# Kernel tuning notes

Hardware: AMD Instinct MI355X
Metric: run time of the kernel (lower is better)

## Reference

```python
import jax, jax.numpy as jnp
import numpy as np
from jax import lax

BN_EPS = 1e-5


def setup_inputs() -> dict:
    key = jax.random.key(0)
    ks = jax.random.split(key, 4)
    T, N, I, H, O, K = 2048, 16, 1024, 2048, 1024, 12
    return {
        "inputs": jax.random.normal(ks[0], (T, N, I), dtype=jnp.float32),
        "wv": jax.random.normal(ks[1], (H, I), dtype=jnp.float32) * (1.0 / np.sqrt(I)),
        "gamma": jnp.ones((H,), dtype=jnp.float32),
        "beta": jnp.zeros((H,), dtype=jnp.float32),
        "wu": jax.random.normal(ks[2], (O, H), dtype=jnp.float32) * (1.0 / np.sqrt(H)),
        "bu": jnp.zeros((O,), dtype=jnp.float32),
        "memory_weights": jax.random.normal(ks[3], (K, H), dtype=jnp.float32) * 0.05,
        "stride": 2,
        "l_memory_size": 10,
        "r_memory_size": 1,
    }


def _memory_block(p, memory_weights, stride, l_mem, r_mem):
    # p: [N, T, H]. p_hatt[n,t,h] = sum_k w[k,h] * p[n, t + (k-l_mem)*stride, h]
    # == depthwise 1D cross-correlation with dilation=stride, 'same' asymmetric pad.
    H = p.shape[-1]
    x = jnp.transpose(p, (0, 2, 1))              # [N, H, T]
    kern = memory_weights.T[:, None, :]          # [H, 1, K]
    out = lax.conv_general_dilated(
        x, kern,
        window_strides=(1,),
        padding=[(l_mem * stride, r_mem * stride)],
        rhs_dilation=(stride,),
        dimension_numbers=("NCH", "OIH", "NCH"),
        feature_group_count=H,
    )
    return jnp.transpose(out, (0, 2, 1))         # [N, T, H]


def reference(inputs, wv, gamma, beta, wu, bu, memory_weights,
              stride, l_memory_size, r_memory_size):
    # wx_v then transpose(0,1): [T,N,I] -> [N,T,H]
    p = jnp.einsum("tni,hi->nth", inputs, wv)
    p_hatt = p + _memory_block(p, memory_weights, stride, l_memory_size, r_memory_size)
    # SequenceWise(BatchNorm1d) in train mode: stats over flattened (N*T) rows.
    H = p_hatt.shape[-1]
    flat = p_hatt.reshape(-1, H)
    mean = flat.mean(axis=0)
    var = flat.var(axis=0)  # biased, matches torch BN normalization
    xn = (p_hatt - mean) * lax.rsqrt(var + BN_EPS) * gamma + beta
    h = jax.nn.relu(jnp.einsum("nth,oh->nto", xn, wu) + bu)
    return (h, p_hatt)
```

## Files before the change

### kernel.cpp

```cpp
#include <hip/hip_runtime.h>
#include <hip/hip_bf16.h>
#include <stdint.h>

#define T_DIM 2048
#define N_DIM 16
#define I_DIM 1024
#define H_DIM 2048
#define O_DIM 1024
#define K_TAPS 12
#define MROWS (N_DIM * T_DIM)
#define BN_EPS 1e-5f

#define S_LEN 1024
#define CSTEPS 16
#define CROWS 27
#define CGROUP 2

typedef __attribute__((ext_vector_type(8))) short bf16x8;
typedef __attribute__((ext_vector_type(4))) float f32x4;

__device__ __forceinline__ unsigned short f2bf_rne(float f) {
    union { float f; unsigned u; } v; v.f = f;
    unsigned u = v.u;
    unsigned r = u + 0x7fffu + ((u >> 16) & 1u);
    return (unsigned short)(r >> 16);
}

__device__ __forceinline__ float bf2f(unsigned short x) {
    union { unsigned u; float f; } v; v.u = ((unsigned)x) << 16; return v.f;
}

__global__ void cvt_kernel(const float* __restrict__ in, unsigned short* __restrict__ out, int n4) {
    int i = blockIdx.x * blockDim.x + threadIdx.x;
    int stride = gridDim.x * blockDim.x;
    for (; i < n4; i += stride) {
        float4 v = ((const float4*)in)[i];
        ushort4 o;
        o.x = f2bf_rne(v.x); o.y = f2bf_rne(v.y);
        o.z = f2bf_rne(v.z); o.w = f2bf_rne(v.w);
        ((ushort4*)out)[i] = o;
    }
}

__device__ __forceinline__ void gload_lds16(const void* g, void* l) {
    __builtin_amdgcn_global_load_lds(
        (const __attribute__((address_space(1))) unsigned int*)g,
        (__attribute__((address_space(3))) unsigned int*)l, 16, 0, 0);
}

template<int PERM, int EPI, int KD, int NCOLS>
__global__ __launch_bounds__(512, 2) void gemm256(
    const unsigned short* __restrict__ A,
    const unsigned short* __restrict__ B,
    void* __restrict__ Cout,
    const float* __restrict__ bias)
{
    __shared__ char lds[131072];

    const int tid  = threadIdx.x;
    const int wid  = tid >> 6;
    const int lane = tid & 63;
    const int wr   = (wid >> 2) * 128;
    const int wc   = (wid & 3) * 64;
    const int fr   = lane & 15;
    const int fh   = lane >> 4;

    const int nwg = gridDim.x;
    const int lin = blockIdx.x;
    const int tile = (lin & 7) * (nwg >> 3) + (lin >> 3);
    const int ntx = NCOLS / 256;
    const long c0 = (long)(tile % ntx) * 256;
    const long r0 = (long)(tile / ntx) * 256;

    long aBase, aStride;
    if (PERM) {
        const long n0 = r0 / T_DIM;
        const long t0 = r0 % T_DIM;
        aBase = (t0 * N_DIM + n0) * (long)KD;
        aStride = (long)N_DIM * KD;
    } else {
        aBase = r0 * (long)KD;
        aStride = KD;
    }
    const long bBase = c0 * (long)KD;

    auto stage_half = [&](int buf, int mat, int h, int kt) {
        char* mbase = lds + buf * 65536 + mat * 32768 + h * 16384;
#pragma unroll
        for (int j = 0; j < 2; ++j) {
            const int row = h * 128 + j * 64 + (tid >> 3);
            const int g   = (tid & 7) ^ (row & 7);
            long gelem;
            if (mat == 0) gelem = aBase + (long)row * aStride + (long)kt * 64 + g * 8;
            else          gelem = bBase + (long)row * (long)KD + (long)kt * 64 + g * 8;
            gload_lds16((const char*)(mat == 0 ? A : B) + gelem * 2,
                        mbase + j * 8192 + tid * 16);
        }
    };

    auto rdA = [&](int buf, int m, int ks) -> bf16x8 {
        const int row = wr + m * 16 + fr;
        const int blk = ks * 4 + fh;
        return *(const bf16x8*)(lds + buf * 65536 + row * 128 + ((blk ^ (row & 7)) << 4));
    };
    auto rdB = [&](int buf, int n, int ks) -> bf16x8 {
        const int row = wc + n * 16 + fr;
        const int blk = ks * 4 + fh;
        return *(const bf16x8*)(lds + buf * 65536 + 32768 + row * 128 + ((blk ^ (row & 7)) << 4));
    };

    f32x4 acc[8][4] = {};

    stage_half(0, 0, 0, 0); stage_half(0, 0, 1, 0);
    stage_half(0, 1, 0, 0); stage_half(0, 1, 1, 0);

    const int KT  = KD / 64;
    const int KT2 = KT / 2;
    for (int i = 0; i < KT2; ++i) {
        const int tB = 2 * i + 1;
        const bool haveNext = (i + 1 < KT2);
        bf16x8 bfr[4][2];

#pragma unroll
        for (int q = 0; q < 4; ++q) {
            stage_half(1, q >> 1, q & 1, tB);
            bf16x8 af[2][2];
            if (q == 0) {
                asm volatile("s_waitcnt vmcnt(2)" ::: "memory");
                __builtin_amdgcn_s_barrier();
#pragma unroll
                for (int n = 0; n < 4; ++n)
#pragma unroll
                    for (int ks = 0; ks < 2; ++ks) bfr[n][ks] = rdB(0, n, ks);
#pragma unroll
                for (int mm = 0; mm < 2; ++mm)
#pragma unroll
                    for (int ks = 0; ks < 2; ++ks) af[mm][ks] = rdA(0, q * 2 + mm, ks);
            } else {
#pragma unroll
                for (int mm = 0; mm < 2; ++mm)
#pragma unroll
                    for (int ks = 0; ks < 2; ++ks) af[mm][ks] = rdA(0, q * 2 + mm, ks);
                __builtin_amdgcn_s_barrier();
            }
            __builtin_amdgcn_s_setprio(1);
#pragma unroll
            for (int mm = 0; mm < 2; ++mm)
#pragma unroll
                for (int n = 0; n < 4; ++n)
#pragma unroll
                    for (int ks = 0; ks < 2; ++ks)
                        acc[q * 2 + mm][n] = __builtin_amdgcn_mfma_f32_16x16x32_bf16(
                            af[mm][ks], bfr[n][ks], acc[q * 2 + mm][n], 0, 0, 0);
            __builtin_amdgcn_s_setprio(0);
            __builtin_amdgcn_s_barrier();
        }

#pragma unroll
        for (int q = 0; q < 4; ++q) {
            if (haveNext) stage_half(0, q >> 1, q & 1, 2 * i + 2);
            bf16x8 af[2][2];
            if (q == 0) {
                if (haveNext) asm volatile("s_waitcnt vmcnt(2)" ::: "memory");
                else          asm volatile("s_waitcnt vmcnt(0)" ::: "memory");
                __builtin_amdgcn_s_barrier();
#pragma unroll
                for (int n = 0; n < 4; ++n)
#pragma unroll
                    for (int ks = 0; ks < 2; ++ks) bfr[n][ks] = rdB(1, n, ks);
#pragma unroll
                for (int mm = 0; mm < 2; ++mm)
#pragma unroll
                    for (int ks = 0; ks < 2; ++ks) af[mm][ks] = rdA(1, q * 2 + mm, ks);
            } else {
#pragma unroll
                for (int mm = 0; mm < 2; ++mm)
#pragma unroll
                    for (int ks = 0; ks < 2; ++ks) af[mm][ks] = rdA(1, q * 2 + mm, ks);
                __builtin_amdgcn_s_barrier();
            }
            __builtin_amdgcn_s_setprio(1);
#pragma unroll
            for (int mm = 0; mm < 2; ++mm)
#pragma unroll
                for (int n = 0; n < 4; ++n)
#pragma unroll
                    for (int ks = 0; ks < 2; ++ks)
                        acc[q * 2 + mm][n] = __builtin_amdgcn_mfma_f32_16x16x32_bf16(
                            af[mm][ks], bfr[n][ks], acc[q * 2 + mm][n], 0, 0, 0);
            __builtin_amdgcn_s_setprio(0);
            __builtin_amdgcn_s_barrier();
        }
    }

#pragma unroll
    for (int m = 0; m < 8; ++m) {
        const long orow_base = r0 + wr + m * 16 + fh * 4;
#pragma unroll
        for (int n = 0; n < 4; ++n) {
            const long ocol = c0 + wc + n * 16 + fr;
#pragma unroll
            for (int j = 0; j < 4; ++j) {
                const long orow = orow_base + j;
                float vv = acc[m][n][j];
                if (EPI == 0) {
                    ((unsigned short*)Cout)[orow * NCOLS + ocol] = f2bf_rne(vv);
                } else {
                    vv += bias[ocol];
                    vv = vv > 0.f ? vv : 0.f;
                    ((float*)Cout)[orow * NCOLS + ocol] = vv;
                }
            }
        }
    }
}

__global__ __launch_bounds__(256, 2) void conv_bn_v5(
    const unsigned short* __restrict__ p,
    const float* __restrict__ w,
    float* __restrict__ ph_f32,
    unsigned short* __restrict__ ph_b,
    float* __restrict__ sums)
{
    const int tid   = threadIdx.x;
    const int b     = blockIdx.x;
    const int half  = b & 1;
    const int grp   = (b >> 1) & 31;
    const int np    = b >> 6;
    const int par   = np & 1;
    const int n     = np >> 1;
    const int h0    = half * 1024 + tid * 4;

    float wk[12][4];
#pragma unroll
    for (int k = 0; k < 12; ++k) {
        float4 v = *(const float4*)&w[k * H_DIM + h0];
        wk[k][0] = v.x; wk[k][1] = v.y; wk[k][2] = v.z; wk[k][3] = v.w;
    }

    const long b0 = ((long)n * T_DIM + par) * (long)H_DIM + h0;

    float st1[4] = {0.f, 0.f, 0.f, 0.f};
    float st2[4] = {0.f, 0.f, 0.f, 0.f};

#pragma unroll 1
    for (int c = 0; c < CGROUP; ++c) {
        const int s0 = (grp * CGROUP + c) * CSTEPS;

        float f[CROWS][4];
#pragma unroll
        for (int j = 0; j < CROWS; ++j) {
            const int s = s0 + j - 10;
            if (s >= 0 && s < S_LEN) {
                ushort4 v = *(const ushort4*)&p[b0 + (long)s * (2 * H_DIM)];
                f[j][0] = bf2f(v.x); f[j][1] = bf2f(v.y);
                f[j][2] = bf2f(v.z); f[j][3] = bf2f(v.w);
            } else {
                f[j][0] = 0.f; f[j][1] = 0.f; f[j][2] = 0.f; f[j][3] = 0.f;
            }
        }

#pragma unroll
        for (int u = 0; u < CSTEPS; ++u) {
            float out[4];
#pragma unroll
            for (int cc = 0; cc < 4; ++cc) out[cc] = f[u + 10][cc];
#pragma unroll
            for (int k = 0; k < 12; ++k)
#pragma unroll
                for (int cc = 0; cc < 4; ++cc)
                    out[cc] += wk[k][cc] * f[u + k][cc];

            const long base = b0 + (long)(s0 + u) * (2 * H_DIM);
            *(float4*)&ph_f32[base] = make_float4(out[0], out[1], out[2], out[3]);
            ushort4 ob;
            ob.x = f2bf_rne(out[0]); ob.y = f2bf_rne(out[1]);
            ob.z = f2bf_rne(out[2]); ob.w = f2bf_rne(out[3]);
            *(ushort4*)&ph_b[base] = ob;
#pragma unroll
            for (int cc = 0; cc < 4; ++cc) { st1[cc] += out[cc]; st2[cc] += out[cc] * out[cc]; }
        }
    }

#pragma unroll
    for (int cc = 0; cc < 4; ++cc) {
        atomicAdd(&sums[h0 + cc], st1[cc]);
        atomicAdd(&sums[H_DIM + h0 + cc], st2[cc]);
    }
}

__global__ void bn_finalize(const float* __restrict__ sums,
                            const float* __restrict__ gamma,
                            const float* __restrict__ beta,
                            float* __restrict__ sshift) {
    int h = blockIdx.x * blockDim.x + threadIdx.x;
    if (h >= H_DIM) return;
    float mean = sums[h] * (1.f / (float)MROWS);
    float var  = sums[H_DIM + h] * (1.f / (float)MROWS) - mean * mean;
    float s = gamma[h] * rsqrtf(var + BN_EPS);
    sshift[h] = s;
    sshift[H_DIM + h] = beta[h] - mean * s;
}

__global__ void scale_wu(const float* __restrict__ wu,
                         const float* __restrict__ sshift,
                         unsigned short* __restrict__ wu2) {
    int idx = blockIdx.x * blockDim.x + threadIdx.x;
    int stride = gridDim.x * blockDim.x;
    for (; idx < O_DIM * H_DIM; idx += stride) {
        int h = idx & (H_DIM - 1);
        wu2[idx] = f2bf_rne(wu[idx] * sshift[h]);
    }
}

__global__ __launch_bounds__(256) void bias2_kernel(
    const float* __restrict__ wu,
    const float* __restrict__ sshift,
    const float* __restrict__ bu,
    float* __restrict__ bias2) {
    const int o = blockIdx.x;
    float part = 0.f;
    for (int h = threadIdx.x; h < H_DIM; h += 256)
        part += sshift[H_DIM + h] * wu[(long)o * H_DIM + h];
#pragma unroll
    for (int off = 32; off > 0; off >>= 1) part += __shfl_down(part, off, 64);
    __shared__ float red[4];
    const int wv = threadIdx.x >> 6, lane = threadIdx.x & 63;
    if (lane == 0) red[wv] = part;
    __syncthreads();
    if (threadIdx.x == 0) bias2[o] = bu[o] + red[0] + red[1] + red[2] + red[3];
}

extern "C" void kernel_launch(void* const* d_in, const int* in_sizes, int n_in,
                              void* d_out, int out_size, void* d_ws, size_t ws_size,
                              hipStream_t stream) {
    const float* inputs = (const float*)d_in[0];
    const float* wv     = (const float*)d_in[1];
    const float* gamma  = (const float*)d_in[2];
    const float* beta   = (const float*)d_in[3];
    const float* wu     = (const float*)d_in[4];
    const float* bu     = (const float*)d_in[5];
    const float* mw     = (const float*)d_in[6];

    float* out_h  = (float*)d_out;
    float* out_ph = out_h + (size_t)MROWS * O_DIM;

    unsigned short* p_b = (unsigned short*)d_out;

    char* ws = (char*)d_ws;
    unsigned short* ph_b  = (unsigned short*)ws;
    unsigned short* in_b  = (unsigned short*)(ws + 134217728);
    unsigned short* wv_b  = (unsigned short*)(ws + 201326592);
    unsigned short* wu2_b = (unsigned short*)(ws + 205520896);
    float* sums   = (float*)(ws + 209715200);
    float* sshift = (float*)(ws + 209731584);
    float* bias2  = (float*)(ws + 209747968);

    hipMemsetAsync(sums, 0, 2 * H_DIM * sizeof(float), stream);

    cvt_kernel<<<2048, 256, 0, stream>>>(inputs, in_b, (T_DIM * N_DIM * I_DIM) / 4);
    cvt_kernel<<<512, 256, 0, stream>>>(wv, wv_b, (H_DIM * I_DIM) / 4);

    gemm256<1, 0, I_DIM, H_DIM><<<(MROWS / 256) * (H_DIM / 256), 512, 0, stream>>>(
        in_b, wv_b, (void*)p_b, nullptr);

    conv_bn_v5<<<2 * 32 * 2 * N_DIM, 256, 0, stream>>>(p_b, mw, out_ph, ph_b, sums);

    bn_finalize<<<(H_DIM + 255) / 256, 256, 0, stream>>>(sums, gamma, beta, sshift);
    scale_wu<<<2048, 256, 0, stream>>>(wu, sshift, wu2_b);
    bias2_kernel<<<O_DIM, 256, 0, stream>>>(wu, sshift, bu, bias2);

    gemm256<0, 1, H_DIM, O_DIM><<<(MROWS / 256) * (O_DIM / 256), 512, 0, stream>>>(
        ph_b, wu2_b, (void*)out_h, bias2);
}
```

Before: 473.4 us.

## Fuse first GEMM with dilated depthwise conv and BN stats using halo rows

```diff
diff --git a/kernel.cpp b/kernel.cpp
--- a/kernel.cpp
+++ b/kernel.cpp
@@ -10,11 +10,6 @@
 #define K_TAPS 12
 #define MROWS (N_DIM * T_DIM)
 #define BN_EPS 1e-5f
-
-#define S_LEN 1024
-#define CSTEPS 16
-#define CROWS 27
-#define CGROUP 2
 
 typedef __attribute__((ext_vector_type(8))) short bf16x8;
 typedef __attribute__((ext_vector_type(4))) float f32x4;
@@ -46,6 +41,237 @@
     __builtin_amdgcn_global_load_lds(
         (const __attribute__((address_space(1))) unsigned int*)g,
         (__attribute__((address_space(3))) unsigned int*)l, 16, 0, 0);
+}
+
+__global__ __launch_bounds__(512, 2) void gemm1_conv(
+    const unsigned short* __restrict__ A,
+    const unsigned short* __restrict__ B,
+    const float* __restrict__ w,
+    float* __restrict__ ph_f32,
+    unsigned short* __restrict__ ph_b,
+    float* __restrict__ sums)
+{
+    __shared__ char lds[148480];
+
+    const int tid  = threadIdx.x;
+    const int wid  = tid >> 6;
+    const int lane = tid & 63;
+    const int wr   = (wid >> 2) * 160;
+    const int wc   = (wid & 3) * 64;
+    const int fr   = lane & 15;
+    const int fh   = lane >> 4;
+
+    const int nwg = gridDim.x;
+    const int lin = blockIdx.x;
+    const int tile = (lin & 7) * (nwg >> 3) + (lin >> 3);
+    const int ntx = H_DIM / 256;
+    const long c0 = (long)(tile % ntx) * 256;
+    const long r0 = (long)(tile / ntx) * 256;
+    const int n0 = (int)(r0 / T_DIM);
+    const int t0 = (int)(r0 % T_DIM);
+
+    const long bBase = c0 * I_DIM;
+
+    auto stageA = [&](int buf, int ci, int kt) {
+        const int lr = ci * 64 + (tid >> 3);
+        int t = t0 - 32 + lr;
+        t = t < 0 ? 0 : (t >= T_DIM ? T_DIM - 1 : t);
+        const int g = (tid & 7) ^ (lr & 7);
+        const long gelem = ((long)t * N_DIM + n0) * I_DIM + kt * 64 + g * 8;
+        gload_lds16((const char*)A + gelem * 2, lds + buf * 40960 + ci * 8192 + tid * 16);
+    };
+    auto stageB2 = [&](int buf, int si, int kt) {
+        const int row = si * 64 + (tid >> 3);
+        const int g = (tid & 7) ^ (row & 7);
+        const long gelem = bBase + (long)row * I_DIM + kt * 64 + g * 8;
+        gload_lds16((const char*)B + gelem * 2, lds + 81920 + buf * 32768 + si * 8192 + tid * 16);
+    };
+    auto rdA = [&](int buf, int m, int ks) -> bf16x8 {
+        const int row = wr + m * 16 + fr;
+        const int blk = ks * 4 + fh;
+        return *(const bf16x8*)(lds + buf * 40960 + row * 128 + ((blk ^ (row & 7)) << 4));
+    };
+    auto rdB = [&](int buf, int n, int ks) -> bf16x8 {
+        const int row = wc + n * 16 + fr;
+        const int blk = ks * 4 + fh;
+        return *(const bf16x8*)(lds + 81920 + buf * 32768 + row * 128 + ((blk ^ (row & 7)) << 4));
+    };
+
+    f32x4 acc[10][4] = {};
+
+    stageA(0, 0, 0); stageA(0, 1, 0); stageA(0, 2, 0); stageA(0, 3, 0); stageA(0, 4, 0);
+    stageB2(0, 0, 0); stageB2(0, 1, 0); stageB2(0, 2, 0); stageB2(0, 3, 0);
+
+    for (int i = 0; i < 8; ++i) {
+        const int tB = 2 * i + 1;
+        const bool haveNext = (i + 1 < 8);
+
+        {
+            bf16x8 bfr[4][2];
+#pragma unroll
+            for (int q = 0; q < 4; ++q) {
+                if (q == 0)      { stageA(1, 0, tB); stageA(1, 1, tB); stageA(1, 2, tB); }
+                else if (q == 1) { stageA(1, 3, tB); stageA(1, 4, tB); stageB2(1, 0, tB); }
+                else if (q == 2) { stageB2(1, 1, tB); stageB2(1, 2, tB); }
+                else             { stageB2(1, 3, tB); }
+                const int ms = (q == 0) ? 0 : (q == 1) ? 3 : (q == 2) ? 6 : 8;
+                const int mc = (q <= 1) ? 3 : 2;
+                bf16x8 af[3][2];
+                if (q == 0) {
+                    asm volatile("s_waitcnt vmcnt(3)" ::: "memory");
+                    __builtin_amdgcn_s_barrier();
+#pragma unroll
+                    for (int n = 0; n < 4; ++n)
+#pragma unroll
+                        for (int ks = 0; ks < 2; ++ks) bfr[n][ks] = rdB(0, n, ks);
+#pragma unroll
+                    for (int mm = 0; mm < 3; ++mm)
+#pragma unroll
+                        for (int ks = 0; ks < 2; ++ks) af[mm][ks] = rdA(0, ms + mm, ks);
+                } else {
+#pragma unroll
+                    for (int mm = 0; mm < 3; ++mm)
+                        if (mm < mc)
+#pragma unroll
+                            for (int ks = 0; ks < 2; ++ks) af[mm][ks] = rdA(0, ms + mm, ks);
+                    __builtin_amdgcn_s_barrier();
+                }
+                __builtin_amdgcn_s_setprio(1);
+#pragma unroll
+                for (int mm = 0; mm < 3; ++mm)
+                    if (mm < mc)
+#pragma unroll
+                        for (int n = 0; n < 4; ++n)
+#pragma unroll
+                            for (int ks = 0; ks < 2; ++ks)
+                                acc[ms + mm][n] = __builtin_amdgcn_mfma_f32_16x16x32_bf16(
+                                    af[mm][ks], bfr[n][ks], acc[ms + mm][n], 0, 0, 0);
+                __builtin_amdgcn_s_setprio(0);
+                __builtin_amdgcn_s_barrier();
+            }
+        }
+
+        {
+            const int tN = 2 * i + 2;
+            bf16x8 bfr[4][2];
+#pragma unroll
+            for (int q = 0; q < 4; ++q) {
+                if (haveNext) {
+                    if (q == 0)      { stageA(0, 0, tN); stageA(0, 1, tN); stageA(0, 2, tN); }
+                    else if (q == 1) { stageA(0, 3, tN); stageA(0, 4, tN); stageB2(0, 0, tN); }
+                    else if (q == 2) { stageB2(0, 1, tN); stageB2(0, 2, tN); }
+                    else             { stageB2(0, 3, tN); }
+                }
+                const int ms = (q == 0) ? 0 : (q == 1) ? 3 : (q == 2) ? 6 : 8;
+                const int mc = (q <= 1) ? 3 : 2;
+                bf16x8 af[3][2];
+                if (q == 0) {
+                    if (haveNext) asm volatile("s_waitcnt vmcnt(3)" ::: "memory");
+                    else          asm volatile("s_waitcnt vmcnt(0)" ::: "memory");
+                    __builtin_amdgcn_s_barrier();
+#pragma unroll
+                    for (int n = 0; n < 4; ++n)
+#pragma unroll
+                        for (int ks = 0; ks < 2; ++ks) bfr[n][ks] = rdB(1, n, ks);
+#pragma unroll
+                    for (int mm = 0; mm < 3; ++mm)
+#pragma unroll
+                        for (int ks = 0; ks < 2; ++ks) af[mm][ks] = rdA(1, ms + mm, ks);
+                } else {
+#pragma unroll
+                    for (int mm = 0; mm < 3; ++mm)
+                        if (mm < mc)
+#pragma unroll
+                            for (int ks = 0; ks < 2; ++ks) af[mm][ks] = rdA(1, ms + mm, ks);
+                    __builtin_amdgcn_s_barrier();
+                }
+                __builtin_amdgcn_s_setprio(1);
+#pragma unroll
+                for (int mm = 0; mm < 3; ++mm)
+                    if (mm < mc)
+#pragma unroll
+                        for (int n = 0; n < 4; ++n)
+#pragma unroll
+                            for (int ks = 0; ks < 2; ++ks)
+                                acc[ms + mm][n] = __builtin_amdgcn_mfma_f32_16x16x32_bf16(
+                                    af[mm][ks], bfr[n][ks], acc[ms + mm][n], 0, 0, 0);
+                __builtin_amdgcn_s_setprio(0);
+                __builtin_amdgcn_s_barrier();
+            }
+        }
+    }
+
+#pragma unroll
+    for (int m = 0; m < 10; ++m) {
+        const int rb = wr + m * 16 + fh * 4;
+        if (rb >= 12 && rb < 290) {
+#pragma unroll
+            for (int n = 0; n < 4; ++n) {
+                const int col = wc + n * 16 + fr;
+                unsigned lo = (unsigned)f2bf_rne(acc[m][n][0]) |
+                              ((unsigned)f2bf_rne(acc[m][n][1]) << 16);
+                unsigned hi = (unsigned)f2bf_rne(acc[m][n][2]) |
+                              ((unsigned)f2bf_rne(acc[m][n][3]) << 16);
+                char* base = lds + col * 564 + (rb - 12) * 2;
+                *(unsigned*)base = lo;
+                *(unsigned*)(base + 4) = hi;
+            }
+        }
+    }
+    __syncthreads();
+
+    {
+        const int col   = tid & 255;
+        const int rhalf = tid >> 8;
+        const long hcol = c0 + col;
+        const char* pcol = lds + col * 564;
+
+        float wkk[12];
+#pragma unroll
+        for (int k = 0; k < 12; ++k) wkk[k] = w[k * H_DIM + hcol];
+
+        float s1 = 0.f, s2 = 0.f;
+#pragma unroll 1
+        for (int par = 0; par < 2; ++par) {
+            const int tcs = rhalf * 128 + par;
+            float win[12];
+#pragma unroll
+            for (int j = 0; j < 12; ++j) {
+                const int dt = (j - 10) * 2;
+                const int tg = t0 + tcs + dt;
+                const int e  = 20 + tcs + dt;
+                win[j] = ((unsigned)tg < T_DIM)
+                         ? bf2f(*(const unsigned short*)(pcol + e * 2)) : 0.f;
+            }
+#pragma unroll
+            for (int u = 0; u < 64; ++u) {
+                const int cr = tcs + 2 * u;
+                float out = win[(u + 10) % 12];
+#pragma unroll
+                for (int k = 0; k < 12; ++k) out += wkk[k] * win[(u + k) % 12];
+
+                const long base = (r0 + cr) * (long)H_DIM + hcol;
+                ph_f32[base] = out;
+                ph_b[base] = f2bf_rne(out);
+                s1 += out; s2 += out * out;
+
+                if (u < 63) {
+                    const int tg2 = t0 + cr + 4;
+                    const int e2  = 20 + cr + 4;
+                    win[u % 12] = ((unsigned)tg2 < T_DIM)
+                                  ? bf2f(*(const unsigned short*)(pcol + e2 * 2)) : 0.f;
+                }
+            }
+        }
+
+        *(float2*)(lds + 144384 + tid * 8) = make_float2(s1, s2);
+        __syncthreads();
+        if (tid < 256) {
+            float2 o = *(const float2*)(lds + 144384 + (tid + 256) * 8);
+            atomicAdd(&sums[hcol], s1 + o.x);
+            atomicAdd(&sums[H_DIM + hcol], s2 + o.y);
+        }
+    }
 }
 
 template<int PERM, int EPI, int KD, int NCOLS>
@@ -212,80 +438,6 @@
                 }
             }
         }
-    }
-}
-
-__global__ __launch_bounds__(256, 2) void conv_bn_v5(
-    const unsigned short* __restrict__ p,
-    const float* __restrict__ w,
-    float* __restrict__ ph_f32,
-    unsigned short* __restrict__ ph_b,
-    float* __restrict__ sums)
-{
-    const int tid   = threadIdx.x;
-    const int b     = blockIdx.x;
-    const int half  = b & 1;
-    const int grp   = (b >> 1) & 31;
-    const int np    = b >> 6;
-    const int par   = np & 1;
-    const int n     = np >> 1;
-    const int h0    = half * 1024 + tid * 4;
-
-    float wk[12][4];
-#pragma unroll
-    for (int k = 0; k < 12; ++k) {
-        float4 v = *(const float4*)&w[k * H_DIM + h0];
-        wk[k][0] = v.x; wk[k][1] = v.y; wk[k][2] = v.z; wk[k][3] = v.w;
-    }
-
-    const long b0 = ((long)n * T_DIM + par) * (long)H_DIM + h0;
-
-    float st1[4] = {0.f, 0.f, 0.f, 0.f};
-    float st2[4] = {0.f, 0.f, 0.f, 0.f};
-
-#pragma unroll 1
-    for (int c = 0; c < CGROUP; ++c) {
-        const int s0 = (grp * CGROUP + c) * CSTEPS;
-
-        float f[CROWS][4];
-#pragma unroll
-        for (int j = 0; j < CROWS; ++j) {
-            const int s = s0 + j - 10;
-            if (s >= 0 && s < S_LEN) {
-                ushort4 v = *(const ushort4*)&p[b0 + (long)s * (2 * H_DIM)];
-                f[j][0] = bf2f(v.x); f[j][1] = bf2f(v.y);
-                f[j][2] = bf2f(v.z); f[j][3] = bf2f(v.w);
-            } else {
-                f[j][0] = 0.f; f[j][1] = 0.f; f[j][2] = 0.f; f[j][3] = 0.f;
-            }
-        }
-
-#pragma unroll
-        for (int u = 0; u < CSTEPS; ++u) {
-            float out[4];
-#pragma unroll
-            for (int cc = 0; cc < 4; ++cc) out[cc] = f[u + 10][cc];
-#pragma unroll
-            for (int k = 0; k < 12; ++k)
-#pragma unroll
-                for (int cc = 0; cc < 4; ++cc)
-                    out[cc] += wk[k][cc] * f[u + k][cc];
-
-            const long base = b0 + (long)(s0 + u) * (2 * H_DIM);
-            *(float4*)&ph_f32[base] = make_float4(out[0], out[1], out[2], out[3]);
-            ushort4 ob;
-            ob.x = f2bf_rne(out[0]); ob.y = f2bf_rne(out[1]);
-            ob.z = f2bf_rne(out[2]); ob.w = f2bf_rne(out[3]);
-            *(ushort4*)&ph_b[base] = ob;
-#pragma unroll
-            for (int cc = 0; cc < 4; ++cc) { st1[cc] += out[cc]; st2[cc] += out[cc] * out[cc]; }
-        }
-    }
-
-#pragma unroll
-    for (int cc = 0; cc < 4; ++cc) {
-        atomicAdd(&sums[h0 + cc], st1[cc]);
-        atomicAdd(&sums[H_DIM + h0 + cc], st2[cc]);
     }
 }
 
@@ -345,8 +497,6 @@
     float* out_h  = (float*)d_out;
     float* out_ph = out_h + (size_t)MROWS * O_DIM;
 
-    unsigned short* p_b = (unsigned short*)d_out;
-
     char* ws = (char*)d_ws;
     unsigned short* ph_b  = (unsigned short*)ws;
     unsigned short* in_b  = (unsigned short*)(ws + 134217728);
@@ -361,10 +511,8 @@
     cvt_kernel<<<2048, 256, 0, stream>>>(inputs, in_b, (T_DIM * N_DIM * I_DIM) / 4);
     cvt_kernel<<<512, 256, 0, stream>>>(wv, wv_b, (H_DIM * I_DIM) / 4);
 
-    gemm256<1, 0, I_DIM, H_DIM><<<(MROWS / 256) * (H_DIM / 256), 512, 0, stream>>>(
-        in_b, wv_b, (void*)p_b, nullptr);
-
-    conv_bn_v5<<<2 * 32 * 2 * N_DIM, 256, 0, stream>>>(p_b, mw, out_ph, ph_b, sums);
+    gemm1_conv<<<(MROWS / 256) * (H_DIM / 256), 512, 0, stream>>>(
+        in_b, wv_b, mw, out_ph, ph_b, sums);
 
     bn_finalize<<<(H_DIM + 255) / 256, 256, 0, stream>>>(sums, gamma, beta, sshift);
     scale_wu<<<2048, 256, 0, stream>>>(wu, sshift, wu2_b);
```

After: 491.9 us. 3.9% more time.
